# Performance work log

Hardware: AMD Instinct MI355X
Metric: run time of the kernel (lower is better)

Reference implementation:

```python
import jax, jax.numpy as jnp
import numpy as np

# Module config (matches init_kwargs)
IC, OC = 8, 16
KH, KW = 3, 3
H, W = 32, 32
PAD, STRIDE = 1, 1
PH, PW = H + 2 * PAD, W + 2 * PAD          # padded input dims: 34x34
OH = (PH - KH) // STRIDE + 1                # 32
OW = (PW - KW) // STRIDE + 1                # 32
B = 64                                       # batch of flattened ciphertext images


def _build_toeplitz(kernel: np.ndarray) -> np.ndarray:
    """approximate_toeplitz_multiple_channels: dense [OC*OH*OW, IC*PH*PW] matrix
    such that T @ vec(padded_x) == vec(conv2d(x, kernel))."""
    T = np.zeros((OC * OH * OW, IC * PH * PW), dtype=np.float32)
    oh, ow = np.meshgrid(np.arange(OH), np.arange(OW), indexing="ij")
    oh, ow = oh.ravel(), ow.ravel()
    for oc in range(OC):
        rows = (oc * OH + oh) * OW + ow
        for ic in range(IC):
            for kh in range(KH):
                for kw in range(KW):
                    cols = (ic * PH + oh * STRIDE + kh) * PW + (ow * STRIDE + kw)
                    T[rows, cols] = kernel[oc, ic, kh, kw]
    return T


def _build_pad_mat() -> np.ndarray:
    """create_padding_transformation_matrix: [IC*PH*PW, IC*H*W] 0/1 matrix that
    zero-pads the flattened image (homomorphic padding as a matmul)."""
    P = np.zeros((IC * PH * PW, IC * H * W), dtype=np.float32)
    ic, h, w = np.meshgrid(np.arange(IC), np.arange(H), np.arange(W), indexing="ij")
    rows = (ic * PH + h + PAD) * PW + (w + PAD)
    cols = (ic * H + h) * W + w
    P[rows.ravel(), cols.ravel()] = 1.0
    return P


def setup_inputs() -> dict:
    rng = np.random.default_rng(0)
    kernel = rng.standard_normal((OC, IC, KH, KW)).astype(np.float32)
    weight = jnp.asarray(_build_toeplitz(kernel))                 # [OC*OH*OW, IC*PH*PW]
    bias = jnp.asarray(
        np.repeat(rng.standard_normal(OC).astype(np.float32), OH * OW)
    )                                                             # [OC*OH*OW]
    pad_mat = jnp.asarray(_build_pad_mat())                       # [IC*PH*PW, IC*H*W]
    key = jax.random.key(0)
    enc_x = jax.random.normal(key, (B, IC * H * W), dtype=jnp.float32)
    return {"enc_x": enc_x, "weight": weight, "bias": bias, "pad_mat": pad_mat}


def reference(enc_x, weight, bias, pad_mat):
    # Homomorphic conv as plaintext-equivalent math:
    # 1) pad via transformation matrix, 2) Toeplitz matmul, 3) add repeated bias.
    x_padded = enc_x @ pad_mat.T            # [B, IC*PH*PW]
    return x_padded @ weight.T + bias       # [B, OC*OH*OW]
```

## Files before the change

### kernel.cpp

```cpp
#include <hip/hip_runtime.h>

#define IC    8
#define OC    16
#define H     32
#define W     32
#define PH    34
#define PW    34
#define OH    32
#define OW    32
#define BATCH 64
#define WCOLS (IC * PH * PW)
#define XSTR  35
#define PLANE (PH * XSTR)

__global__ __launch_bounds__(256) void conv_toeplitz_kernel(
    const float* __restrict__ x,
    const float* __restrict__ weight,
    const float* __restrict__ bias,
    float* __restrict__ out)
{
    __shared__ float wk[IC * 9];
    __shared__ float xs[IC * PLANE];

    const int tid = threadIdx.x;
    const int blk = blockIdx.x;
    const int b   = blk >> 4;
    const int oc  = blk & 15;

    if (tid < IC * 9) {
        const int ic = tid / 9;
        const int k  = tid - ic * 9;
        const int kh = k / 3;
        const int kw = k - kh * 3;
        wk[tid] = weight[(size_t)(oc * OH * OW) * WCOLS + (ic * PH + kh) * PW + kw];
    }

    for (int i = tid; i < IC * PLANE; i += 256) xs[i] = 0.0f;
    __syncthreads();

    const float4* xg = (const float4*)(x + (size_t)b * (IC * H * W));
    #pragma unroll
    for (int i = 0; i < 8; ++i) {
        const int k   = tid + i * 256;
        const float4 v = xg[k];
        const int ic  = k >> 8;
        const int rem = k & 255;
        const int h   = rem >> 3;
        const int w4  = (rem & 7) << 2;
        float* dst = &xs[ic * PLANE + (h + 1) * XSTR + (w4 + 1)];
        dst[0] = v.x; dst[1] = v.y; dst[2] = v.z; dst[3] = v.w;
    }
    __syncthreads();

    float wreg[IC][3][3];
    #pragma unroll
    for (int ic = 0; ic < IC; ++ic)
        #pragma unroll
        for (int kh = 0; kh < 3; ++kh)
            #pragma unroll
            for (int kw = 0; kw < 3; ++kw)
                wreg[ic][kh][kw] = wk[ic * 9 + kh * 3 + kw];

    const int oh   = tid >> 3;
    const int ow0  = (tid & 7) << 2;
    const int oidx = oh * OW + ow0;

    const float4 bv = *(const float4*)(bias + oc * OH * OW + oidx);
    float acc0 = bv.x, acc1 = bv.y, acc2 = bv.z, acc3 = bv.w;

    #pragma unroll
    for (int ic = 0; ic < IC; ++ic) {
        #pragma unroll
        for (int kh = 0; kh < 3; ++kh) {
            const float* row = &xs[ic * PLANE + (oh + kh) * XSTR + ow0];
            const float v0 = row[0], v1 = row[1], v2 = row[2];
            const float v3 = row[3], v4 = row[4], v5 = row[5];
            const float w0 = wreg[ic][kh][0];
            const float w1 = wreg[ic][kh][1];
            const float w2 = wreg[ic][kh][2];
            acc0 += v0 * w0 + v1 * w1 + v2 * w2;
            acc1 += v1 * w0 + v2 * w1 + v3 * w2;
            acc2 += v2 * w0 + v3 * w1 + v4 * w2;
            acc3 += v3 * w0 + v4 * w1 + v5 * w2;
        }
    }

    float* op = out + (size_t)(b * OC + oc) * (OH * OW) + oidx;
    *(float4*)op = make_float4(acc0, acc1, acc2, acc3);
}

extern "C" void kernel_launch(void* const* d_in, const int* in_sizes, int n_in,
                              void* d_out, int out_size, void* d_ws, size_t ws_size,
                              hipStream_t stream) {
    const float* x      = (const float*)d_in[0];
    const float* weight = (const float*)d_in[1];
    const float* bias   = (const float*)d_in[2];
    float* out = (float*)d_out;

    conv_toeplitz_kernel<<<dim3(BATCH * OC), dim3(256), 0, stream>>>(x, weight, bias, out);
}
```

Measured before the change: 12.78 us.

## Compute two output channels per block and zero only padding border

Each block now computes two output channels for one batch image, so every staged input plane in shared memory feeds twice as many outputs and the block count is halved. Only the one-element padding border of shared memory is zeroed, which removes one barrier. Kernel weights are read directly from global memory into registers rather than staged through shared memory. Launch bounds now request two blocks per CU, which raises register pressure from the doubled accumulators and weights and halves the available grid parallelism.

Measured after the change: 11.39 us. -10.9%, faster.

```diff
diff --git a/kernel.cpp b/kernel.cpp
--- a/kernel.cpp
+++ b/kernel.cpp
@@ -6,42 +6,39 @@
 #define W     32
 #define PH    34
 #define PW    34
-#define OH    32
-#define OW    32
 #define BATCH 64
 #define WCOLS (IC * PH * PW)
 #define XSTR  35
 #define PLANE (PH * XSTR)
 
-__global__ __launch_bounds__(256) void conv_toeplitz_kernel(
+__global__ __launch_bounds__(256, 2) void conv_v8_kernel(
     const float* __restrict__ x,
     const float* __restrict__ weight,
     const float* __restrict__ bias,
     float* __restrict__ out)
 {
-    __shared__ float wk[IC * 9];
     __shared__ float xs[IC * PLANE];
 
     const int tid = threadIdx.x;
     const int blk = blockIdx.x;
-    const int b   = blk >> 4;
-    const int oc  = blk & 15;
+    const int b   = blk >> 3;
+    const int oc0 = (blk & 7) << 1;
 
-    if (tid < IC * 9) {
-        const int ic = tid / 9;
-        const int k  = tid - ic * 9;
-        const int kh = k / 3;
-        const int kw = k - kh * 3;
-        wk[tid] = weight[(size_t)(oc * OH * OW) * WCOLS + (ic * PH + kh) * PW + kw];
+    for (int i = tid; i < IC * 132; i += 256) {
+        const int p = i / 132;
+        const int r = i - p * 132;
+        int row, col;
+        if (r < 34)       { row = 0;       col = r;      }
+        else if (r < 68)  { row = 33;      col = r - 34; }
+        else if (r < 100) { row = r - 67;  col = 0;      }
+        else              { row = r - 99;  col = 33;     }
+        xs[p * PLANE + row * XSTR + col] = 0.0f;
     }
-
-    for (int i = tid; i < IC * PLANE; i += 256) xs[i] = 0.0f;
-    __syncthreads();
 
     const float4* xg = (const float4*)(x + (size_t)b * (IC * H * W));
     #pragma unroll
     for (int i = 0; i < 8; ++i) {
-        const int k   = tid + i * 256;
+        const int k   = tid + (i << 8);
         const float4 v = xg[k];
         const int ic  = k >> 8;
         const int rem = k & 255;
@@ -52,41 +49,54 @@
     }
     __syncthreads();
 
-    float wreg[IC][3][3];
+    const float* wp0 = weight + (size_t)(oc0 << 10) * WCOLS;
+    const float* wp1 = wp0 + ((size_t)1024) * WCOLS;
+
+    const int oh   = tid >> 3;
+    const int ow0  = (tid & 7) << 2;
+    const int oidx = (oh << 5) + ow0;
+
+    const float4 b0 = *(const float4*)(bias + (oc0 << 10) + oidx);
+    const float4 b1 = *(const float4*)(bias + ((oc0 + 1) << 10) + oidx);
+    float a00 = b0.x, a01 = b0.y, a02 = b0.z, a03 = b0.w;
+    float a10 = b1.x, a11 = b1.y, a12 = b1.z, a13 = b1.w;
+
     #pragma unroll
-    for (int ic = 0; ic < IC; ++ic)
+    for (int ic = 0; ic < IC; ++ic) {
+        float wA[9], wB[9];
         #pragma unroll
         for (int kh = 0; kh < 3; ++kh)
             #pragma unroll
-            for (int kw = 0; kw < 3; ++kw)
-                wreg[ic][kh][kw] = wk[ic * 9 + kh * 3 + kw];
+            for (int kw = 0; kw < 3; ++kw) {
+                wA[kh * 3 + kw] = wp0[(ic * PH + kh) * PW + kw];
+                wB[kh * 3 + kw] = wp1[(ic * PH + kh) * PW + kw];
+            }
 
-    const int oh   = tid >> 3;
-    const int ow0  = (tid & 7) << 2;
-    const int oidx = oh * OW + ow0;
-
-    const float4 bv = *(const float4*)(bias + oc * OH * OW + oidx);
-    float acc0 = bv.x, acc1 = bv.y, acc2 = bv.z, acc3 = bv.w;
-
-    #pragma unroll
-    for (int ic = 0; ic < IC; ++ic) {
         #pragma unroll
         for (int kh = 0; kh < 3; ++kh) {
             const float* row = &xs[ic * PLANE + (oh + kh) * XSTR + ow0];
             const float v0 = row[0], v1 = row[1], v2 = row[2];
             const float v3 = row[3], v4 = row[4], v5 = row[5];
-            const float w0 = wreg[ic][kh][0];
-            const float w1 = wreg[ic][kh][1];
-            const float w2 = wreg[ic][kh][2];
-            acc0 += v0 * w0 + v1 * w1 + v2 * w2;
-            acc1 += v1 * w0 + v2 * w1 + v3 * w2;
-            acc2 += v2 * w0 + v3 * w1 + v4 * w2;
-            acc3 += v3 * w0 + v4 * w1 + v5 * w2;
+            {
+                const float w0 = wA[kh * 3], w1 = wA[kh * 3 + 1], w2 = wA[kh * 3 + 2];
+                a00 += v0 * w0 + v1 * w1 + v2 * w2;
+                a01 += v1 * w0 + v2 * w1 + v3 * w2;
+                a02 += v2 * w0 + v3 * w1 + v4 * w2;
+                a03 += v3 * w0 + v4 * w1 + v5 * w2;
+            }
+            {
+                const float w0 = wB[kh * 3], w1 = wB[kh * 3 + 1], w2 = wB[kh * 3 + 2];
+                a10 += v0 * w0 + v1 * w1 + v2 * w2;
+                a11 += v1 * w0 + v2 * w1 + v3 * w2;
+                a12 += v2 * w0 + v3 * w1 + v4 * w2;
+                a13 += v3 * w0 + v4 * w1 + v5 * w2;
+            }
         }
     }
 
-    float* op = out + (size_t)(b * OC + oc) * (OH * OW) + oidx;
-    *(float4*)op = make_float4(acc0, acc1, acc2, acc3);
+    float* o0 = out + (size_t)(((b << 4) + oc0) << 10) + oidx;
+    *(float4*)o0          = make_float4(a00, a01, a02, a03);
+    *(float4*)(o0 + 1024) = make_float4(a10, a11, a12, a13);
 }
 
 extern "C" void kernel_launch(void* const* d_in, const int* in_sizes, int n_in,
@@ -97,5 +107,5 @@
     const float* bias   = (const float*)d_in[2];
     float* out = (float*)d_out;
 
-    conv_toeplitz_kernel<<<dim3(BATCH * OC), dim3(256), 0, stream>>>(x, weight, bias, out);
+    conv_v8_kernel<<<dim3(BATCH * 8), dim3(256), 0, stream>>>(x, weight, bias, out);
 }
```
